# Performance work log

Hardware: AMD Instinct MI355X
Metric: run time of the kernel (lower is better)

The kernel has to match this reference:

```python
import jax, jax.numpy as jnp
import numpy as np

# ---- static config (matches init_kwargs) ----
B, CIN, H, W = 32, 64, 32, 32
CO, K, G, PAD = 64, 7, 8, 3
R_RAMP = 3.0            # ramp size R
Z_INIT = 4.0            # initial adaptive-span value
MAXSZ = W // 2          # adaptive_mask max_size = image_size/2 = 16
CPG = CO // G           # channels per group


def _unfold(t, k):
    # torch x.unfold(2,k,1).unfold(3,k,1): [B,C,Hp,Wp] -> [B,C,Ho,Wo,kh,kw]
    ho = t.shape[2] - k + 1
    wo = t.shape[3] - k + 1
    return jnp.stack(
        [jnp.stack([t[:, :, i:i + ho, j:j + wo] for j in range(k)], axis=-1)
         for i in range(k)], axis=-2)


def _adaptive_mask(current_val):
    # AdaptiveMask.forward applied to [B,G,CPG,H,W]; x.shape[-1] == W.
    # one_d_mask[g, i] is the soft value written on 'ring' i (rows i and W-1-i,
    # columns spanning the ring interval) of a WxW mask.
    template = jnp.linspace(1.0 - MAXSZ, 0.0, MAXSZ)            # [MAXSZ]
    om = (template[None, :] + current_val * MAXSZ) / R_RAMP + 1.0
    om = jnp.clip(om, 0.0, 1.0)                                  # [G, MAXSZ]
    # (slice [-(W//2):] is identity since MAXSZ == W//2)
    i = jnp.arange(W)
    r = jnp.minimum(i, W - 1 - i)                                # ring index per row
    top = i <= (W - 1 - i)
    lo = jnp.where(top, r, r + 1)    # bottom row of ring misses its leftmost col
    hi = W - 1 - r
    c = jnp.arange(W)
    in_ring = (c[None, :] >= lo[:, None]) & (c[None, :] <= hi[:, None])  # [W,W]
    vals = om[:, r]                                              # [G, W]
    return jnp.where(in_ring[None, :, :], vals[:, :, None], 1.0)  # [G,W,W]


def setup_inputs() -> dict:
    key = jax.random.key(0)
    ks = jax.random.split(key, 6)
    x = jax.random.normal(ks[0], (B, CIN, H, W), dtype=jnp.float32)
    fan_out_std = np.sqrt(2.0 / CO).astype(np.float32)  # kaiming fan_out, 1x1 conv
    w_q = jax.random.normal(ks[1], (CO, CIN), dtype=jnp.float32) * fan_out_std
    w_k = jax.random.normal(ks[2], (CO, CIN), dtype=jnp.float32) * fan_out_std
    w_v = jax.random.normal(ks[3], (CO, CIN), dtype=jnp.float32) * fan_out_std
    rel_h = jax.random.normal(ks[4], (CO // 2, 1, 1, K, 1), dtype=jnp.float32)
    rel_w = jax.random.normal(ks[5], (CO // 2, 1, 1, 1, K), dtype=jnp.float32)
    current_val = jnp.full((G, 1), Z_INIT, dtype=jnp.float32)
    return {"x": x, "w_q": w_q, "w_k": w_k, "w_v": w_v,
            "rel_h": rel_h, "rel_w": rel_w, "current_val": current_val}


def reference(x, w_q, w_k, w_v, rel_h, rel_w, current_val):
    q = jnp.einsum('bchw,oc->bohw', x, w_q)                       # [B,CO,H,W]
    xp = jnp.pad(x, ((0, 0), (0, 0), (PAD, PAD), (PAD, PAD)))
    k = jnp.einsum('bchw,oc->bohw', xp, w_k)
    v = jnp.einsum('bchw,oc->bohw', xp, w_v)
    k = _unfold(k, K)                                             # [B,CO,H,W,K,K]
    v = _unfold(v, K)
    k_h, k_w = jnp.split(k, 2, axis=1)
    k = jnp.concatenate([k_h + rel_h, k_w + rel_w], axis=1)
    k = k.reshape(B, G, CPG, H, W, K * K)
    v = v.reshape(B, G, CPG, H, W, K * K)
    q = q.reshape(B, G, CPG, H, W, 1)
    scores = jnp.sum(q * k, axis=2)                               # [B,G,H,W,K*K]
    attn = jax.nn.softmax(scores, axis=-1)
    out = jnp.sum(attn[:, :, None] * v, axis=-1)                  # [B,G,CPG,H,W]
    mask = _adaptive_mask(current_val)                            # [G,W,W]
    return out * mask[None, :, None, :, :]
```

## Files before the change

### kernel.cpp

```cpp
#include <hip/hip_runtime.h>

#define BB    32
#define CINc  64
#define HHc   32
#define WWc   32
#define COc   64
#define KSc   7
#define GGc   8
#define PADc  3
#define CPGc  8
#define NPIX  (HHc * WWc)
#define TILEH 16
#define HALOH (TILEH + 6)
#define HALOW (WWc + 6)
#define NPOS  (HALOH * HALOW)
#define NVALID (19 * 32)
#define NPAD   (NPOS - NVALID)

__global__ __launch_bounds__(512, 4) void fused_kernel(
    const float* __restrict__ x,
    const float* __restrict__ wq,
    const float* __restrict__ wk,
    const float* __restrict__ wv,
    const float* __restrict__ rel_h,
    const float* __restrict__ rel_w,
    const float* __restrict__ cv,
    float* __restrict__ out)
{
    __shared__ __attribute__((aligned(16))) float4 kvp[4][NPOS];

    const int bi   = blockIdx.x;
    const int t    = bi >> 3;
    const int j    = t & 15;
    const int b    = (t >> 4) * 8 + (bi & 7);
    const int g    = j >> 1;
    const int tile = j & 1;
    const int o0   = g * CPGc;
    const int tid  = threadIdx.x;

    const int y0  = tile * TILEH - PADc;
    const int yv0 = (tile == 0) ? 0 : y0;
    const int r0  = yv0 - y0;
    const float* xb = x + (size_t)b * CINc * NPIX;

    if (tid < NPAD) {
        int r, cc;
        if (tid < 114) {
            const int rb = (tile == 0) ? 0 : 19;
            r  = rb + tid / 38;
            cc = tid % 38;
        } else {
            const int tt = tid - 114;
            const int c6 = tt % 6;
            r  = r0 + tt / 6;
            cc = (c6 < 3) ? c6 : (c6 + 32);
        }
        const int p = r * HALOW + cc;
        const float4 z = {0.f, 0.f, 0.f, 0.f};
        kvp[0][p] = z; kvp[1][p] = z; kvp[2][p] = z; kvp[3][p] = z;
    }

#pragma unroll 1
    for (int i = tid; i < NVALID; i += 512) {
        const int row = i >> 5;
        const int xx  = i & 31;
        const int y   = yv0 + row;
        const int r   = r0 + row;
        const float* xp = xb + y * WWc + xx;

        float ak[CPGc], av[CPGc];
#pragma unroll
        for (int oi = 0; oi < CPGc; ++oi) { ak[oi] = 0.f; av[oi] = 0.f; }

        for (int c0 = 0; c0 < CINc; c0 += 8) {
            float xv[8];
#pragma unroll
            for (int jj = 0; jj < 8; ++jj)
                xv[jj] = xp[(c0 + jj) * NPIX];
#pragma unroll
            for (int oi = 0; oi < CPGc; ++oi) {
                const float* wkr = wk + (o0 + oi) * CINc + c0;
                const float* wvr = wv + (o0 + oi) * CINc + c0;
#pragma unroll
                for (int jj = 0; jj < 8; ++jj) {
                    ak[oi] = fmaf(xv[jj], wkr[jj], ak[oi]);
                    av[oi] = fmaf(xv[jj], wvr[jj], av[oi]);
                }
            }
        }

        const int p = r * HALOW + (xx + PADc);
        kvp[0][p] = (float4){ak[0], ak[1], ak[2], ak[3]};
        kvp[1][p] = (float4){ak[4], ak[5], ak[6], ak[7]};
        kvp[2][p] = (float4){av[0], av[1], av[2], av[3]};
        kvp[3][p] = (float4){av[4], av[5], av[6], av[7]};
    }

    const int w  = tid & 31;
    const int lh = tid >> 5;
    const int h  = tile * TILEH + lh;
    const int poff = h * WWc + w;

    float q[CPGc];
#pragma unroll
    for (int oi = 0; oi < CPGc; ++oi) q[oi] = 0.f;

    for (int c0 = 0; c0 < CINc; c0 += 8) {
        float xv[8];
#pragma unroll
        for (int jj = 0; jj < 8; ++jj)
            xv[jj] = xb[(c0 + jj) * NPIX + poff];
#pragma unroll
        for (int oi = 0; oi < CPGc; ++oi) {
            const float* wqr = wq + (o0 + oi) * CINc + c0;
#pragma unroll
            for (int jj = 0; jj < 8; ++jj)
                q[oi] = fmaf(xv[jj], wqr[jj], q[oi]);
        }
    }

    const bool use_h = (g < 4);
    const float* relp = use_h ? (rel_h + o0 * KSc) : (rel_w + (o0 - 32) * KSc);
    float qrel[KSc];
#pragma unroll
    for (int tt = 0; tt < KSc; ++tt) {
        float s = 0.f;
#pragma unroll
        for (int oi = 0; oi < CPGc; ++oi)
            s = fmaf(q[oi], relp[oi * KSc + tt], s);
        qrel[tt] = s;
    }

    __syncthreads();

    float den = 0.f;
    float acc[CPGc];
#pragma unroll
    for (int oi = 0; oi < CPGc; ++oi) acc[oi] = 0.f;

#pragma unroll
    for (int ki = 0; ki < KSc; ++ki) {
        const int rbase = (lh + ki) * HALOW + w;
#pragma unroll
        for (int kj = 0; kj < KSc; ++kj) {
            const int p = rbase + kj;
            const float4 k0 = kvp[0][p];
            const float4 k1 = kvp[1][p];
            const float4 v0 = kvp[2][p];
            const float4 v1 = kvp[3][p];

            float s = use_h ? qrel[ki] : qrel[kj];
            s = fmaf(q[0], k0.x, s); s = fmaf(q[1], k0.y, s);
            s = fmaf(q[2], k0.z, s); s = fmaf(q[3], k0.w, s);
            s = fmaf(q[4], k1.x, s); s = fmaf(q[5], k1.y, s);
            s = fmaf(q[6], k1.z, s); s = fmaf(q[7], k1.w, s);

            const float e = __expf(s);
            den += e;
            acc[0] = fmaf(e, v0.x, acc[0]); acc[1] = fmaf(e, v0.y, acc[1]);
            acc[2] = fmaf(e, v0.z, acc[2]); acc[3] = fmaf(e, v0.w, acc[3]);
            acc[4] = fmaf(e, v1.x, acc[4]); acc[5] = fmaf(e, v1.y, acc[5]);
            acc[6] = fmaf(e, v1.z, acc[6]); acc[7] = fmaf(e, v1.w, acc[7]);
        }
    }

    const int  r  = min(h, HHc - 1 - h);
    const int  lo = (h <= HHc - 1 - h) ? r : r + 1;
    const int  hi = HHc - 1 - r;
    const bool in_ring = (w >= lo) && (w <= hi);
    const float cvg = cv[g];
    float om = ((float)r - 15.0f + cvg * 16.0f) * (1.0f / 3.0f) + 1.0f;
    om = fminf(fmaxf(om, 0.0f), 1.0f);
    const float maskv = in_ring ? om : 1.0f;
    const float scale = maskv / den;

    float* ob = out + ((size_t)b * COc + o0) * NPIX + poff;
#pragma unroll
    for (int oi = 0; oi < CPGc; ++oi)
        ob[(size_t)oi * NPIX] = acc[oi] * scale;
}

extern "C" void kernel_launch(void* const* d_in, const int* in_sizes, int n_in,
                              void* d_out, int out_size, void* d_ws, size_t ws_size,
                              hipStream_t stream) {
    const float* x     = (const float*)d_in[0];
    const float* wq    = (const float*)d_in[1];
    const float* wk    = (const float*)d_in[2];
    const float* wv    = (const float*)d_in[3];
    const float* rel_h = (const float*)d_in[4];
    const float* rel_w = (const float*)d_in[5];
    const float* cv    = (const float*)d_in[6];
    float* out = (float*)d_out;

    fused_kernel<<<512, 512, 0, stream>>>(x, wq, wk, wv, rel_h, rel_w, cv, out);
}
```

Baseline: 106.3 us.

## Store keys in fp16 with fdot2 scoring and split into smaller row tiles

Keys are packed as fp16 pairs in shared memory, and the q·k score uses the packed fp16 dot-product builtin (v_dot2), which cuts LDS key traffic in half and reduces FMA count. The tile height drops from 16 to 8 rows, and the launch changes to 1024 blocks of 256 threads, which adds occupancy and parallelism. In exchange the halo K/V projection overhead grows, since each block now recomputes a 14-row halo for 8 output rows, and the lower key precision may affect accuracy. Padding is now zeroed with a full clear and an extra barrier.

Result: no change. 106.7 us (+0.3%).

```diff
diff --git a/kernel.cpp b/kernel.cpp
--- a/kernel.cpp
+++ b/kernel.cpp
@@ -10,14 +10,20 @@
 #define PADc  3
 #define CPGc  8
 #define NPIX  (HHc * WWc)
-#define TILEH 16
+#define TILEH 8
 #define HALOH (TILEH + 6)
 #define HALOW (WWc + 6)
 #define NPOS  (HALOH * HALOW)
-#define NVALID (19 * 32)
-#define NPAD   (NPOS - NVALID)
-
-__global__ __launch_bounds__(512, 4) void fused_kernel(
+
+typedef _Float16 half2v __attribute__((ext_vector_type(2)));
+
+#if defined(__has_builtin)
+#if __has_builtin(__builtin_amdgcn_fdot2)
+#define HAVE_FDOT2 1
+#endif
+#endif
+
+__global__ __launch_bounds__(256, 6) void fused_kernel(
     const float* __restrict__ x,
     const float* __restrict__ wq,
     const float* __restrict__ wk,
@@ -27,45 +33,41 @@
     const float* __restrict__ cv,
     float* __restrict__ out)
 {
-    __shared__ __attribute__((aligned(16))) float4 kvp[4][NPOS];
+    __shared__ __attribute__((aligned(16))) float4 kpl[NPOS];
+    __shared__ __attribute__((aligned(16))) float4 vpl0[NPOS];
+    __shared__ __attribute__((aligned(16))) float4 vpl1[NPOS];
 
     const int bi   = blockIdx.x;
-    const int t    = bi >> 3;
-    const int j    = t & 15;
-    const int b    = (t >> 4) * 8 + (bi & 7);
-    const int g    = j >> 1;
-    const int tile = j & 1;
+    const int xcd  = bi & 7;
+    const int sIdx = bi >> 3;
+    const int im   = sIdx >> 5;
+    const int j    = sIdx & 31;
+    const int b    = im * 8 + xcd;
+    const int g    = j >> 2;
+    const int tile = j & 3;
     const int o0   = g * CPGc;
     const int tid  = threadIdx.x;
 
     const int y0  = tile * TILEH - PADc;
-    const int yv0 = (tile == 0) ? 0 : y0;
+    const int yv0 = (y0 < 0) ? 0 : y0;
+    const int yv1 = (y0 + HALOH - 1 > HHc - 1) ? (HHc - 1) : (y0 + HALOH - 1);
+    const int nvp = ((yv1 - yv0) + 1) << 5;
     const int r0  = yv0 - y0;
     const float* xb = x + (size_t)b * CINc * NPIX;
 
-    if (tid < NPAD) {
-        int r, cc;
-        if (tid < 114) {
-            const int rb = (tile == 0) ? 0 : 19;
-            r  = rb + tid / 38;
-            cc = tid % 38;
-        } else {
-            const int tt = tid - 114;
-            const int c6 = tt % 6;
-            r  = r0 + tt / 6;
-            cc = (c6 < 3) ? c6 : (c6 + 32);
-        }
-        const int p = r * HALOW + cc;
+    {
         const float4 z = {0.f, 0.f, 0.f, 0.f};
-        kvp[0][p] = z; kvp[1][p] = z; kvp[2][p] = z; kvp[3][p] = z;
-    }
+        for (int p = tid; p < NPOS; p += 256) {
+            kpl[p] = z; vpl0[p] = z; vpl1[p] = z;
+        }
+    }
+    __syncthreads();
 
 #pragma unroll 1
-    for (int i = tid; i < NVALID; i += 512) {
+    for (int i = tid; i < nvp; i += 256) {
         const int row = i >> 5;
         const int xx  = i & 31;
         const int y   = yv0 + row;
-        const int r   = r0 + row;
         const float* xp = xb + y * WWc + xx;
 
         float ak[CPGc], av[CPGc];
@@ -89,11 +91,15 @@
             }
         }
 
-        const int p = r * HALOW + (xx + PADc);
-        kvp[0][p] = (float4){ak[0], ak[1], ak[2], ak[3]};
-        kvp[1][p] = (float4){ak[4], ak[5], ak[6], ak[7]};
-        kvp[2][p] = (float4){av[0], av[1], av[2], av[3]};
-        kvp[3][p] = (float4){av[4], av[5], av[6], av[7]};
+        const int p = (r0 + row) * HALOW + (xx + PADc);
+        float4 kst;
+        half2v* kp = (half2v*)&kst;
+#pragma unroll
+        for (int jj = 0; jj < 4; ++jj)
+            kp[jj] = half2v{(_Float16)ak[2 * jj], (_Float16)ak[2 * jj + 1]};
+        kpl[p]  = kst;
+        vpl0[p] = (float4){av[0], av[1], av[2], av[3]};
+        vpl1[p] = (float4){av[4], av[5], av[6], av[7]};
     }
 
     const int w  = tid & 31;
@@ -119,6 +125,13 @@
         }
     }
 
+#if HAVE_FDOT2
+    half2v q2[4];
+#pragma unroll
+    for (int jj = 0; jj < 4; ++jj)
+        q2[jj] = half2v{(_Float16)q[2 * jj], (_Float16)q[2 * jj + 1]};
+#endif
+
     const bool use_h = (g < 4);
     const float* relp = use_h ? (rel_h + o0 * KSc) : (rel_w + (o0 - 32) * KSc);
     float qrel[KSc];
@@ -144,17 +157,25 @@
 #pragma unroll
         for (int kj = 0; kj < KSc; ++kj) {
             const int p = rbase + kj;
-            const float4 k0 = kvp[0][p];
-            const float4 k1 = kvp[1][p];
-            const float4 v0 = kvp[2][p];
-            const float4 v1 = kvp[3][p];
+            const float4 kraw = kpl[p];
+            const float4 v0   = vpl0[p];
+            const float4 v1   = vpl1[p];
 
             float s = use_h ? qrel[ki] : qrel[kj];
-            s = fmaf(q[0], k0.x, s); s = fmaf(q[1], k0.y, s);
-            s = fmaf(q[2], k0.z, s); s = fmaf(q[3], k0.w, s);
-            s = fmaf(q[4], k1.x, s); s = fmaf(q[5], k1.y, s);
-            s = fmaf(q[6], k1.z, s); s = fmaf(q[7], k1.w, s);
-
+#if HAVE_FDOT2
+            const half2v* kh = (const half2v*)&kraw;
+            s = __builtin_amdgcn_fdot2(q2[0], kh[0], s, false);
+            s = __builtin_amdgcn_fdot2(q2[1], kh[1], s, false);
+            s = __builtin_amdgcn_fdot2(q2[2], kh[2], s, false);
+            s = __builtin_amdgcn_fdot2(q2[3], kh[3], s, false);
+#else
+            const half2v* kh = (const half2v*)&kraw;
+#pragma unroll
+            for (int jj = 0; jj < 4; ++jj) {
+                s = fmaf(q[2 * jj],     (float)kh[jj].x, s);
+                s = fmaf(q[2 * jj + 1], (float)kh[jj].y, s);
+            }
+#endif
             const float e = __expf(s);
             den += e;
             acc[0] = fmaf(e, v0.x, acc[0]); acc[1] = fmaf(e, v0.y, acc[1]);
@@ -192,5 +213,5 @@
     const float* cv    = (const float*)d_in[6];
     float* out = (float*)d_out;
 
-    fused_kernel<<<512, 512, 0, stream>>>(x, wq, wk, wv, rel_h, rel_w, cv, out);
+    fused_kernel<<<1024, 256, 0, stream>>>(x, wq, wk, wv, rel_h, rel_w, cv, out);
 }
```
